# Kernel tuning notes

Hardware: AMD Instinct MI355X
Metric: run time of the kernel (lower is better)

The kernel has to match this reference:

```python
import jax, jax.numpy as jnp
import numpy as np

DIM = 1024
N_HEAD = 16
N_KV_HEAD = 4
HEAD_DIM = DIM // N_HEAD  # 64
INTER = 2688
B, N = 2, 2048
EPS = 1e-6


def setup_inputs() -> dict:
    key = jax.random.key(0)
    ks = jax.random.split(key, 10)
    std = 0.02
    x = jax.random.normal(ks[0], (B, N, DIM), dtype=jnp.float32)
    # rotary embedding: theta = pos * 10000^(-2i/d), cos/sin of shape [N, HEAD_DIM//2]
    inv_freq = 1.0 / (10000.0 ** (np.arange(0, HEAD_DIM, 2, dtype=np.float32) / HEAD_DIM))
    t = np.arange(N, dtype=np.float32)
    ang = np.outer(t, inv_freq)  # [N, HEAD_DIM//2]
    rope_cos = jnp.asarray(np.cos(ang))
    rope_sin = jnp.asarray(np.sin(ang))
    mask = jnp.tril(jnp.ones((N, N), dtype=bool))  # True = attend
    return {
        "x": x,
        "w_attn_norm": jnp.ones((DIM,), jnp.float32),
        "w_ffn_norm": jnp.ones((DIM,), jnp.float32),
        "Wq": jax.random.normal(ks[1], (DIM, N_HEAD * HEAD_DIM), jnp.float32) * std,
        "Wkv": jax.random.normal(ks[2], (DIM, 2 * N_KV_HEAD * HEAD_DIM), jnp.float32) * std,
        "Wo": jax.random.normal(ks[3], (N_HEAD * HEAD_DIM, DIM), jnp.float32) * std,
        "W1": jax.random.normal(ks[4], (DIM, INTER), jnp.float32) * std,
        "W2": jax.random.normal(ks[5], (INTER, DIM), jnp.float32) * std,
        "W3": jax.random.normal(ks[6], (DIM, INTER), jnp.float32) * std,
        "rope_cos": rope_cos,
        "rope_sin": rope_sin,
        "mask": mask,
    }


def _rms_norm(x, w):
    # nn.functional.rms_norm: x / sqrt(mean(x^2) + eps) * w
    return x * jax.lax.rsqrt(jnp.mean(x * x, axis=-1, keepdims=True) + EPS) * w


def _apply_rope(x, cos, sin):
    # x: [b, n, h, d]; consecutive pairs (x[2k], x[2k+1]) form complex numbers
    xr = x[..., 0::2]
    xi = x[..., 1::2]
    c = cos[None, :, None, :]
    s = sin[None, :, None, :]
    yr = xr * c - xi * s
    yi = xr * s + xi * c
    return jnp.stack([yr, yi], axis=-1).reshape(x.shape)


def _block(x, w_attn_norm, w_ffn_norm, Wq, Wkv, Wo, W1, W2, W3, rope_cos, rope_sin, mask):
    b, n, _ = x.shape
    # --- attention (GQA, use_cache=False prefill) ---
    h = _rms_norm(x, w_attn_norm)
    q = (h @ Wq).reshape(b, n, N_HEAD, HEAD_DIM)
    kv = h @ Wkv
    k, v = jnp.split(kv, 2, axis=-1)
    k = k.reshape(b, n, N_KV_HEAD, HEAD_DIM)
    v = v.reshape(b, n, N_KV_HEAD, HEAD_DIM)
    q = _apply_rope(q, rope_cos, rope_sin)
    k = _apply_rope(k, rope_cos, rope_sin)
    # einops repeat 'b n h d -> b n (r h) d' == tile along head axis
    r = N_HEAD // N_KV_HEAD
    k = jnp.tile(k, (1, 1, r, 1))
    v = jnp.tile(v, (1, 1, r, 1))
    scale = HEAD_DIM ** -0.5
    scores = jnp.einsum('bnhd,bmhd->bhnm', q, k) * scale
    scores = jnp.where(mask[None, None, :, :], scores, jnp.finfo(scores.dtype).min)
    attn = jax.nn.softmax(scores, axis=-1)
    o = jnp.einsum('bhnm,bmhd->bnhd', attn, v).reshape(b, n, N_HEAD * HEAD_DIM)
    x = x + o @ Wo
    # --- SwiGLU MLP ---
    h2 = _rms_norm(x, w_ffn_norm)
    ff = (jax.nn.silu(h2 @ W1) * (h2 @ W3)) @ W2
    return x + ff


def reference(x, w_attn_norm, w_ffn_norm, Wq, Wkv, Wo, W1, W2, W3, rope_cos, rope_sin, mask):
    return _block(x, w_attn_norm, w_ffn_norm, Wq, Wkv, Wo, W1, W2, W3, rope_cos, rope_sin, mask)
```

## Files before the change

kernel.cpp:

```cpp
#include <hip/hip_runtime.h>

#define DIM 1024
#define NH 16
#define NKV 4
#define HD 64
#define INTER 2688
#define BB 2
#define NN 2048
#define MM (BB*NN)

typedef __attribute__((ext_vector_type(4))) float f32x4;
typedef __attribute__((ext_vector_type(16))) float f32x16;
typedef __attribute__((ext_vector_type(8))) short short8;

#define CROW(r,h) ((((r)&3)) + 8*((r)>>2) + 4*(h))

__device__ __forceinline__ unsigned short f2bf(float f) {
  union { float f; unsigned u; } v; v.f = f;
  unsigned r = v.u + 0x7fffu + ((v.u >> 16) & 1u);
  return (unsigned short)(r >> 16);
}

__device__ __forceinline__ void glds16(const unsigned short* g, unsigned short* l) {
  __builtin_amdgcn_global_load_lds(
      (const __attribute__((address_space(1))) void*)g,
      (__attribute__((address_space(3))) void*)l, 16, 0, 0);
}

__device__ __forceinline__ void xcd_map(int& bx, int& by) {
  int gx = gridDim.x;
  int nwg = gx * gridDim.y;
  int bid = (int)blockIdx.y * gx + (int)blockIdx.x;
  int cpx = nwg >> 3;
  int lg = (bid & 7) * cpx + (bid >> 3);
  bx = lg % gx;
  by = lg / gx;
}

__global__ void transpose_all(const float* __restrict__ Wq, const float* __restrict__ Wkv,
                              const float* __restrict__ Wo, const float* __restrict__ W1,
                              const float* __restrict__ W3, const float* __restrict__ W2,
                              unsigned short* __restrict__ WqkvT, unsigned short* __restrict__ WoT,
                              unsigned short* __restrict__ W1T, unsigned short* __restrict__ W3T,
                              unsigned short* __restrict__ W2T) {
  int tb = blockIdx.x;
  const float* src; unsigned short* dst; int K, Nc, t0;
  if (tb < 1024)        { src = Wq;  dst = WqkvT;                         K = 1024; Nc = 1024; t0 = tb; }
  else if (tb < 1536)   { src = Wkv; dst = WqkvT + (size_t)1024 * 1024;   K = 1024; Nc = 512;  t0 = tb - 1024; }
  else if (tb < 2560)   { src = Wo;  dst = WoT;                           K = 1024; Nc = 1024; t0 = tb - 1536; }
  else if (tb < 5248)   { src = W1;  dst = W1T;                           K = 1024; Nc = 2688; t0 = tb - 2560; }
  else if (tb < 7936)   { src = W3;  dst = W3T;                           K = 1024; Nc = 2688; t0 = tb - 5248; }
  else                  { src = W2;  dst = W2T;                           K = 2688; Nc = 1024; t0 = tb - 7936; }
  int ntx = Nc >> 5;
  int n0 = (t0 % ntx) * 32, k0 = (t0 / ntx) * 32;
  __shared__ float tile[32][33];
  int tx = threadIdx.x & 31, ty = threadIdx.x >> 5;
#pragma unroll
  for (int i = 0; i < 32; i += 8)
    tile[ty + i][tx] = src[(size_t)(k0 + ty + i) * Nc + n0 + tx];
  __syncthreads();
#pragma unroll
  for (int i = 0; i < 32; i += 8)
    dst[(size_t)(n0 + ty + i) * K + k0 + tx] = f2bf(tile[tx][ty + i]);
}

__global__ void rmsnorm_k(const float* __restrict__ x, const float* __restrict__ w,
                          unsigned short* __restrict__ h) {
  int row = blockIdx.x;
  int t = threadIdx.x;
  const float4* xr = (const float4*)(x + (size_t)row * DIM);
  float4 v = xr[t];
  float ss = v.x * v.x + v.y * v.y + v.z * v.z + v.w * v.w;
#pragma unroll
  for (int o = 1; o < 64; o <<= 1) ss += __shfl_xor(ss, o);
  __shared__ float ps[4];
  if ((t & 63) == 0) ps[t >> 6] = ss;
  __syncthreads();
  float r = rsqrtf((ps[0] + ps[1] + ps[2] + ps[3]) * (1.0f / DIM) + 1e-6f);
  const float4* wr = (const float4*)w;
  float4 wv = wr[t];
  ushort4 o4;
  o4.x = f2bf(v.x * r * wv.x);
  o4.y = f2bf(v.y * r * wv.y);
  o4.z = f2bf(v.z * r * wv.z);
  o4.w = f2bf(v.w * r * wv.w);
  *(ushort4*)(h + (size_t)row * DIM + t * 4) = o4;
}

template <bool RES>
__global__ __launch_bounds__(256, 3) void gemm_f32(
    const unsigned short* __restrict__ A, const unsigned short* __restrict__ Bt,
    const float* __restrict__ res, float* __restrict__ C, int Nc, int K) {
  __shared__ __align__(16) unsigned short Asm[3][128 * 32];
  __shared__ __align__(16) unsigned short Bsm[3][128 * 32];
  int tid = threadIdx.x;
  int w = tid >> 6, l = tid & 63;
  int bx, by;
  xcd_map(bx, by);
  int bm = by * 128, bn = bx * 128;
  int wr = (w >> 1) * 64, wc = (w & 1) * 64;
  int c0 = l & 15, g = l >> 4;

  int sr = w * 32 + (l >> 2);
  int sc = ((l & 3) ^ ((sr >> 1) & 3)) * 8;
  const unsigned short* gA0 = A + (size_t)(bm + sr) * K + sc;
  const unsigned short* gA1 = A + (size_t)(bm + sr + 16) * K + sc;
  const unsigned short* gB0 = Bt + (size_t)(bn + sr) * K + sc;
  const unsigned short* gB1 = Bt + (size_t)(bn + sr + 16) * K + sc;
  int ls0 = (w * 32) * 32, ls1 = (w * 32 + 16) * 32;

  int aoff[4], boff[4];
#pragma unroll
  for (int m = 0; m < 4; m++) {
    int ra = wr + m * 16 + c0;
    aoff[m] = ra * 32 + (g ^ ((ra >> 1) & 3)) * 8;
    int rb = wc + m * 16 + c0;
    boff[m] = rb * 32 + (g ^ ((rb >> 1) & 3)) * 8;
  }

  f32x4 acc[4][4] = {};
  int T = K / 32;
  glds16(gA0, &Asm[0][ls0]);
  glds16(gA1, &Asm[0][ls1]);
  glds16(gB0, &Bsm[0][ls0]);
  glds16(gB1, &Bsm[0][ls1]);
  glds16(gA0 + 32, &Asm[1][ls0]);
  glds16(gA1 + 32, &Asm[1][ls1]);
  glds16(gB0 + 32, &Bsm[1][ls0]);
  glds16(gB1 + 32, &Bsm[1][ls1]);
  int cur = 0;
  for (int t = 0; t < T; ++t) {
    if (t + 2 < T) {
      int nx = cur + 2; if (nx >= 3) nx -= 3;
      int ko = (t + 2) * 32;
      glds16(gA0 + ko, &Asm[nx][ls0]);
      glds16(gA1 + ko, &Asm[nx][ls1]);
      glds16(gB0 + ko, &Bsm[nx][ls0]);
      glds16(gB1 + ko, &Bsm[nx][ls1]);
      asm volatile("s_waitcnt vmcnt(8)" ::: "memory");
    } else if (t + 2 == T) {
      asm volatile("s_waitcnt vmcnt(4)" ::: "memory");
    } else {
      asm volatile("s_waitcnt vmcnt(0)" ::: "memory");
    }
    __builtin_amdgcn_s_barrier();
    __builtin_amdgcn_sched_barrier(0);
    const unsigned short* As = Asm[cur];
    const unsigned short* Bs = Bsm[cur];
    short8 af[4], bf[4];
#pragma unroll
    for (int m = 0; m < 4; m++) af[m] = *(const short8*)&As[aoff[m]];
#pragma unroll
    for (int n = 0; n < 4; n++) bf[n] = *(const short8*)&Bs[boff[n]];
    __builtin_amdgcn_s_setprio(1);
#pragma unroll
    for (int m = 0; m < 4; m++)
#pragma unroll
      for (int n = 0; n < 4; n++)
        acc[m][n] = __builtin_amdgcn_mfma_f32_16x16x32_bf16(af[m], bf[n], acc[m][n], 0, 0, 0);
    __builtin_amdgcn_s_setprio(0);
    asm volatile("s_waitcnt lgkmcnt(0)" ::: "memory");
    __builtin_amdgcn_sched_barrier(0);
    __builtin_amdgcn_s_barrier();
    cur = cur + 1 == 3 ? 0 : cur + 1;
  }
  int gq = l >> 4;
#pragma unroll
  for (int m = 0; m < 4; m++) {
#pragma unroll
    for (int i = 0; i < 4; i++) {
      int row = bm + wr + m * 16 + gq * 4 + i;
#pragma unroll
      for (int n = 0; n < 4; n++) {
        int col = bn + wc + n * 16 + c0;
        float v = acc[m][n][i];
        if (RES) v += res[(size_t)row * Nc + col];
        C[(size_t)row * Nc + col] = v;
      }
    }
  }
}

__global__ __launch_bounds__(256, 3) void gemm_qkv(
    const unsigned short* __restrict__ A, const unsigned short* __restrict__ Bt,
    const float* __restrict__ cosb, const float* __restrict__ sinb,
    unsigned short* __restrict__ qb, unsigned short* __restrict__ kb,
    unsigned short* __restrict__ vtb) {
  const int Nc = 1536, K = 1024;
  const float QS = 0.125f * 1.44269504f;
  __shared__ __align__(16) unsigned short Asm[3][128 * 32];
  __shared__ __align__(16) unsigned short Bsm[3][128 * 32];
  int tid = threadIdx.x;
  int w = tid >> 6, l = tid & 63;
  int bx, by;
  xcd_map(bx, by);
  int bm = by * 128, bn = bx * 128;
  int wr = (w >> 1) * 64, wc = (w & 1) * 64;
  int c0 = l & 15, g = l >> 4;

  int sr = w * 32 + (l >> 2);
  int sc = ((l & 3) ^ ((sr >> 1) & 3)) * 8;
  const unsigned short* gA0 = A + (size_t)(bm + sr) * K + sc;
  const unsigned short* gA1 = A + (size_t)(bm + sr + 16) * K + sc;
  const unsigned short* gB0 = Bt + (size_t)(bn + sr) * K + sc;
  const unsigned short* gB1 = Bt + (size_t)(bn + sr + 16) * K + sc;
  int ls0 = (w * 32) * 32, ls1 = (w * 32 + 16) * 32;

  int aoff[4], boff[4];
#pragma unroll
  for (int m = 0; m < 4; m++) {
    int ra = wr + m * 16 + c0;
    aoff[m] = ra * 32 + (g ^ ((ra >> 1) & 3)) * 8;
    int rb = wc + m * 16 + c0;
    boff[m] = rb * 32 + (g ^ ((rb >> 1) & 3)) * 8;
  }

  f32x4 acc[4][4] = {};
  int T = K / 32;
  glds16(gA0, &Asm[0][ls0]);
  glds16(gA1, &Asm[0][ls1]);
  glds16(gB0, &Bsm[0][ls0]);
  glds16(gB1, &Bsm[0][ls1]);
  glds16(gA0 + 32, &Asm[1][ls0]);
  glds16(gA1 + 32, &Asm[1][ls1]);
  glds16(gB0 + 32, &Bsm[1][ls0]);
  glds16(gB1 + 32, &Bsm[1][ls1]);
  int cur = 0;
  for (int t = 0; t < T; ++t) {
    if (t + 2 < T) {
      int nx = cur + 2; if (nx >= 3) nx -= 3;
      int ko = (t + 2) * 32;
      glds16(gA0 + ko, &Asm[nx][ls0]);
      glds16(gA1 + ko, &Asm[nx][ls1]);
      glds16(gB0 + ko, &Bsm[nx][ls0]);
      glds16(gB1 + ko, &Bsm[nx][ls1]);
      asm volatile("s_waitcnt vmcnt(8)" ::: "memory");
    } else if (t + 2 == T) {
      asm volatile("s_waitcnt vmcnt(4)" ::: "memory");
    } else {
      asm volatile("s_waitcnt vmcnt(0)" ::: "memory");
    }
    __builtin_amdgcn_s_barrier();
    __builtin_amdgcn_sched_barrier(0);
    const unsigned short* As = Asm[cur];
    const unsigned short* Bs = Bsm[cur];
    short8 af[4], bf[4];
#pragma unroll
    for (int m = 0; m < 4; m++) af[m] = *(const short8*)&As[aoff[m]];
#pragma unroll
    for (int n = 0; n < 4; n++) bf[n] = *(const short8*)&Bs[boff[n]];
    __builtin_amdgcn_s_setprio(1);
#pragma unroll
    for (int m = 0; m < 4; m++)
#pragma unroll
      for (int n = 0; n < 4; n++)
        acc[m][n] = __builtin_amdgcn_mfma_f32_16x16x32_bf16(af[m], bf[n], acc[m][n], 0, 0, 0);
    __builtin_amdgcn_s_setprio(0);
    asm volatile("s_waitcnt lgkmcnt(0)" ::: "memory");
    __builtin_amdgcn_sched_barrier(0);
    __builtin_amdgcn_s_barrier();
    cur = cur + 1 == 3 ? 0 : cur + 1;
  }
  int gq = l >> 4;
  int lodd = c0 & 1;
#pragma unroll
  for (int m = 0; m < 4; m++) {
#pragma unroll
    for (int i = 0; i < 4; i++) {
      int row = bm + wr + m * 16 + gq * 4 + i;
      int b = row >> 11, tok = row & (NN - 1);
#pragma unroll
      for (int n = 0; n < 4; n++) {
        int col = bn + wc + n * 16 + c0;
        float val = acc[m][n][i];
        float partner = __shfl_xor(val, 1);
        if (bn < 1024) {
          int head = col >> 6, d = col & 63, j = d >> 1;
          float c = cosb[tok * 32 + j], s = sinb[tok * 32 + j];
          float r = lodd ? (partner * s + val * c) : (val * c - partner * s);
          qb[(((size_t)(b * NH + head)) * NN + tok) * 64 + d] = f2bf(r * QS);
        } else if (bn < 1280) {
          int cc = col - 1024;
          int kvh = cc >> 6, d = cc & 63, j = d >> 1;
          float c = cosb[tok * 32 + j], s = sinb[tok * 32 + j];
          float r = lodd ? (partner * s + val * c) : (val * c - partner * s);
          kb[(((size_t)(b * NKV + kvh)) * NN + tok) * 64 + d] = f2bf(r);
        } else {
          int cc = col - 1280;
          int kvh = cc >> 6, d = cc & 63;
          vtb[(((size_t)(b * NKV + kvh)) * 64 + d) * NN + tok] = f2bf(val);
        }
      }
    }
  }
}

__global__ __launch_bounds__(256, 3) void gemm_ffn13(
    const unsigned short* __restrict__ A, const unsigned short* __restrict__ B1t,
    const unsigned short* __restrict__ B3t, unsigned short* __restrict__ G,
    int Nc, int K) {
  __shared__ __align__(16) unsigned short Asm[2 * 128 * 32];
  __shared__ __align__(16) unsigned short B1sm[2 * 64 * 32];
  __shared__ __align__(16) unsigned short B3sm[2 * 64 * 32];
  int tid = threadIdx.x;
  int w = tid >> 6, l = tid & 63;
  int bx, by;
  xcd_map(bx, by);
  int bm = by * 128, bn = bx * 64;
  int wr = (w >> 1) * 64, wc = (w & 1) * 32;
  int c0 = l & 15, g = l >> 4;

  int sr = w * 32 + (l >> 2);
  int sb = w * 16 + (l >> 2);
  int sc  = ((l & 3) ^ ((sr >> 1) & 3)) * 8;
  int scb = ((l & 3) ^ ((sb >> 1) & 3)) * 8;
  const unsigned short* gA0 = A + (size_t)(bm + sr) * K + sc;
  const unsigned short* gA1 = A + (size_t)(bm + sr + 16) * K + sc;
  const unsigned short* gB1 = B1t + (size_t)(bn + sb) * K + scb;
  const unsigned short* gB3 = B3t + (size_t)(bn + sb) * K + scb;
  int ls0 = (w * 32) * 32, ls1 = (w * 32 + 16) * 32, lsb = (w * 16) * 32;

  int aoff[4], boff[2];
#pragma unroll
  for (int m = 0; m < 4; m++) {
    int ra = wr + m * 16 + c0;
    aoff[m] = ra * 32 + (g ^ ((ra >> 1) & 3)) * 8;
  }
#pragma unroll
  for (int n = 0; n < 2; n++) {
    int rb = wc + n * 16 + c0;
    boff[n] = rb * 32 + (g ^ ((rb >> 1) & 3)) * 8;
  }

  f32x4 a1[4][2] = {};
  f32x4 a3[4][2] = {};
  int nsteps = K / 32;
  glds16(gA0, &Asm[ls0]);
  glds16(gA1, &Asm[ls1]);
  glds16(gB1, &B1sm[lsb]);
  glds16(gB3, &B3sm[lsb]);
  __syncthreads();
  int buf = 0;
  for (int s = 0; s < nsteps; ++s) {
    int nb = buf ^ 1;
    if (s + 1 < nsteps) {
      int ko = (s + 1) * 32;
      glds16(gA0 + ko, &Asm[nb * 4096 + ls0]);
      glds16(gA1 + ko, &Asm[nb * 4096 + ls1]);
      glds16(gB1 + ko, &B1sm[nb * 2048 + lsb]);
      glds16(gB3 + ko, &B3sm[nb * 2048 + lsb]);
    }
    const unsigned short* As = &Asm[buf * 4096];
    const unsigned short* B1s = &B1sm[buf * 2048];
    const unsigned short* B3s = &B3sm[buf * 2048];
    short8 af[4], b1f[2], b3f[2];
#pragma unroll
    for (int m = 0; m < 4; m++) af[m] = *(const short8*)&As[aoff[m]];
#pragma unroll
    for (int n = 0; n < 2; n++) {
      b1f[n] = *(const short8*)&B1s[boff[n]];
      b3f[n] = *(const short8*)&B3s[boff[n]];
    }
    __builtin_amdgcn_s_setprio(1);
#pragma unroll
    for (int m = 0; m < 4; m++)
#pragma unroll
      for (int n = 0; n < 2; n++) {
        a1[m][n] = __builtin_amdgcn_mfma_f32_16x16x32_bf16(af[m], b1f[n], a1[m][n], 0, 0, 0);
        a3[m][n] = __builtin_amdgcn_mfma_f32_16x16x32_bf16(af[m], b3f[n], a3[m][n], 0, 0, 0);
      }
    __builtin_amdgcn_s_setprio(0);
    __syncthreads();
    buf = nb;
  }
  int gq = l >> 4;
#pragma unroll
  for (int m = 0; m < 4; m++) {
#pragma unroll
    for (int i = 0; i < 4; i++) {
      int row = bm + wr + m * 16 + gq * 4 + i;
#pragma unroll
      for (int n = 0; n < 2; n++) {
        int col = bn + wc + n * 16 + c0;
        float x1 = a1[m][n][i], x3 = a3[m][n][i];
        float sg = x1 / (1.0f + __expf(-x1));
        G[(size_t)row * Nc + col] = f2bf(sg * x3);
      }
    }
  }
}

__global__ __launch_bounds__(256, 3) void attn_k(
    const unsigned short* __restrict__ qg_, const unsigned short* __restrict__ kg_,
    const unsigned short* __restrict__ vg_, unsigned short* __restrict__ ob) {
  __shared__ __align__(16) unsigned short Ksm[2][64 * 64];
  __shared__ __align__(16) unsigned short Vsm[2][64 * 64];
  int qb = (blockIdx.z == 0) ? (int)blockIdx.x : ((int)gridDim.x - 1 - (int)blockIdx.x);
  int h = blockIdx.y, b = blockIdx.z;
  int kvh = h & 3;
  int tid = threadIdx.x, w = tid >> 6, l = tid & 63;
  int q5 = l & 31, hi = l >> 5;
  int qwbase = qb * 128 + w * 32;
  int qgl = qwbase + q5;

  const unsigned short* Kg = kg_ + ((size_t)(b * NKV + kvh)) * NN * 64;
  const unsigned short* Vg = vg_ + ((size_t)(b * NKV + kvh)) * 64 * NN;

  short8 qf[4];
  {
    const unsigned short* qrow = qg_ + (((size_t)(b * NH + h)) * NN + qgl) * 64 + hi * 8;
#pragma unroll
    for (int d = 0; d < 4; d++) qf[d] = *(const short8*)(qrow + d * 16);
  }

  int srow = l >> 3;
  int schunk = (l & 7) ^ (srow & 7);
  const unsigned short* gK = Kg + (size_t)(w * 16 + srow) * 64 + schunk * 8;
  const unsigned short* gV = Vg + (size_t)(w * 16 + srow) * NN + schunk * 8;

  int nkt = qb * 2 + 2;
  int nkt_w = ((qwbase + 31) >> 6) + 1;

  f32x16 O0 = {}, O1 = {};
  float m_r = -1e30f, l_r = 0.0f;

  glds16(gK, &Ksm[0][w * 1024]);
  glds16(gK + 8 * 64, &Ksm[0][w * 1024 + 512]);
  glds16(gV, &Vsm[0][w * 1024]);
  glds16(gV + 8 * NN, &Vsm[0][w * 1024 + 512]);
  __syncthreads();

  int buf = 0;
  for (int kt = 0; kt < nkt; ++kt) {
    int n0 = kt * 64;
    if (kt + 1 < nkt) {
      int nb = buf ^ 1;
      glds16(gK + (size_t)(n0 + 64) * 64, &Ksm[nb][w * 1024]);
      glds16(gK + (size_t)(n0 + 64) * 64 + 8 * 64, &Ksm[nb][w * 1024 + 512]);
      glds16(gV + n0 + 64, &Vsm[nb][w * 1024]);
      glds16(gV + 8 * NN + n0 + 64, &Vsm[nb][w * 1024 + 512]);
    }
    if (kt < nkt_w) {
      const unsigned short* Ks = Ksm[buf];
      const unsigned short* Vs = Vsm[buf];
      f32x16 S[2];
      __builtin_amdgcn_s_setprio(1);
#pragma unroll
      for (int s = 0; s < 2; s++) {
        f32x16 acc = {};
        int row = s * 32 + q5;
#pragma unroll
        for (int d = 0; d < 4; d++) {
          int ch = (2 * d + hi) ^ (row & 7);
          short8 kf = *(const short8*)&Ks[row * 64 + ch * 8];
          acc = __builtin_amdgcn_mfma_f32_32x32x16_bf16(kf, qf[d], acc, 0, 0, 0);
        }
        S[s] = acc;
      }
      __builtin_amdgcn_s_setprio(0);
      if (kt == nkt_w - 1) {
#pragma unroll
        for (int s = 0; s < 2; s++)
#pragma unroll
          for (int r = 0; r < 16; r++) {
            int kg = n0 + s * 32 + CROW(r, hi);
            S[s][r] = (kg > qgl) ? -1e30f : S[s][r];
          }
      }
      float t16[16];
#pragma unroll
      for (int r = 0; r < 16; r++) t16[r] = fmaxf(S[0][r], S[1][r]);
#pragma unroll
      for (int k = 8; k >= 1; k >>= 1)
#pragma unroll
        for (int r = 0; r < k; r++) t16[r] = fmaxf(t16[r], t16[r + k]);
      float pm = fmaxf(t16[0], __shfl_xor(t16[0], 32));
      if (!__all(pm <= m_r + 8.0f)) {
        float mn = fmaxf(m_r, pm);
        float alpha = exp2f(m_r - mn);
        m_r = mn;
        l_r *= alpha;
        float ab[16];
#pragma unroll
        for (int r = 0; r < 16; r++) ab[r] = __shfl(alpha, CROW(r, 0) + 4 * hi);
#pragma unroll
        for (int r = 0; r < 16; r++) { O0[r] *= ab[r]; O1[r] *= ab[r]; }
      }
#pragma unroll
      for (int s = 0; s < 2; s++)
#pragma unroll
        for (int r = 0; r < 16; r++) S[s][r] = exp2f(S[s][r] - m_r);
      float u[16];
#pragma unroll
      for (int r = 0; r < 16; r++) u[r] = S[0][r] + S[1][r];
#pragma unroll
      for (int k = 8; k >= 1; k >>= 1)
#pragma unroll
        for (int r = 0; r < k; r++) u[r] += u[r + k];
      l_r += (u[0] + __shfl_xor(u[0], 32));
      short8 paf[4];
#pragma unroll
      for (int ks = 0; ks < 4; ks++) {
        const int s = ks >> 1, e = ks & 1;
        unsigned a0, a1, b0, b1;
        asm("v_cvt_pk_bf16_f32 %0, %1, %2" : "=v"(a0) : "v"(S[s][8*e+0]), "v"(S[s][8*e+1]));
        asm("v_cvt_pk_bf16_f32 %0, %1, %2" : "=v"(a1) : "v"(S[s][8*e+2]), "v"(S[s][8*e+3]));
        asm("v_cvt_pk_bf16_f32 %0, %1, %2" : "=v"(b0) : "v"(S[s][8*e+4]), "v"(S[s][8*e+5]));
        asm("v_cvt_pk_bf16_f32 %0, %1, %2" : "=v"(b1) : "v"(S[s][8*e+6]), "v"(S[s][8*e+7]));
        asm("v_permlane32_swap_b32 %0, %1" : "+v"(a0), "+v"(b0));
        asm("v_permlane32_swap_b32 %0, %1" : "+v"(a1), "+v"(b1));
        union { unsigned u4[4]; short8 s8; } pk;
        pk.u4[0] = a0; pk.u4[1] = a1; pk.u4[2] = b0; pk.u4[3] = b1;
        paf[ks] = pk.s8;
      }
      __builtin_amdgcn_s_setprio(1);
#pragma unroll
      for (int ks = 0; ks < 4; ks++) {
        int row0 = q5, row1 = 32 + q5;
        short8 vf0 = *(const short8*)&Vs[row0 * 64 + (((2 * ks + hi) ^ (row0 & 7)) * 8)];
        short8 vf1 = *(const short8*)&Vs[row1 * 64 + (((2 * ks + hi) ^ (row1 & 7)) * 8)];
        O0 = __builtin_amdgcn_mfma_f32_32x32x16_bf16(paf[ks], vf0, O0, 0, 0, 0);
        O1 = __builtin_amdgcn_mfma_f32_32x32x16_bf16(paf[ks], vf1, O1, 0, 0, 0);
      }
      __builtin_amdgcn_s_setprio(0);
    }
    __syncthreads();
    buf ^= 1;
  }
  float linv = 1.0f / l_r;
  float lb[16];
#pragma unroll
  for (int r = 0; r < 16; r++) lb[r] = __shfl(linv, CROW(r, 0) + 4 * hi);
#pragma unroll
  for (int r = 0; r < 16; r++) {
    int orow = qwbase + CROW(r, hi);
    size_t base = ((size_t)b * NN + orow) * 1024 + h * 64 + q5;
    ob[base] = f2bf(O0[r] * lb[r]);
    ob[base + 32] = f2bf(O1[r] * lb[r]);
  }
}

extern "C" void kernel_launch(void* const* d_in, const int* in_sizes, int n_in,
                              void* d_out, int out_size, void* d_ws, size_t ws_size,
                              hipStream_t stream) {
  (void)in_sizes; (void)n_in; (void)out_size; (void)ws_size;
  const float* x    = (const float*)d_in[0];
  const float* w_an = (const float*)d_in[1];
  const float* w_fn = (const float*)d_in[2];
  const float* Wq   = (const float*)d_in[3];
  const float* Wkv  = (const float*)d_in[4];
  const float* Wo   = (const float*)d_in[5];
  const float* W1   = (const float*)d_in[6];
  const float* W2   = (const float*)d_in[7];
  const float* W3   = (const float*)d_in[8];
  const float* cosb = (const float*)d_in[9];
  const float* sinb = (const float*)d_in[10];
  float* out = (float*)d_out;

  char* ws = (char*)d_ws;
  size_t off = 0;
  auto take = [&](size_t bytes) {
    size_t r = off;
    off += (bytes + 255) & ~(size_t)255;
    return r;
  };
  unsigned short* WqkvT = (unsigned short*)(ws + take((size_t)1536 * 1024 * 2));
  unsigned short* WoT   = (unsigned short*)(ws + take((size_t)1024 * 1024 * 2));
  unsigned short* W1T   = (unsigned short*)(ws + take((size_t)2688 * 1024 * 2));
  unsigned short* W3T   = (unsigned short*)(ws + take((size_t)2688 * 1024 * 2));
  unsigned short* W2T   = (unsigned short*)(ws + take((size_t)2688 * 1024 * 2));
  unsigned short* hA    = (unsigned short*)(ws + take((size_t)MM * DIM * 2));
  unsigned short* gbuf  = (unsigned short*)(ws + take((size_t)MM * INTER * 2));
  unsigned short* qbuf = (unsigned short*)(ws + take((size_t)MM * DIM * 2));
  unsigned short* kbuf = (unsigned short*)(ws + take((size_t)BB * NKV * NN * HD * 2));
  unsigned short* vtb  = (unsigned short*)(ws + take((size_t)BB * NKV * NN * HD * 2));
  unsigned short* obuf = (unsigned short*)(ws + take((size_t)MM * DIM * 2));
  float* x2 = (float*)(ws + take((size_t)MM * DIM * 4));

  transpose_all<<<10624, 256, 0, stream>>>(Wq, Wkv, Wo, W1, W3, W2,
                                           WqkvT, WoT, W1T, W3T, W2T);
  rmsnorm_k<<<MM, 256, 0, stream>>>(x, w_an, hA);
  gemm_qkv<<<dim3(1536 / 128, MM / 128), 256, 0, stream>>>(hA, WqkvT, cosb, sinb,
                                                           qbuf, kbuf, vtb);
  attn_k<<<dim3(NN / 128, NH, BB), 256, 0, stream>>>(qbuf, kbuf, vtb, obuf);
  gemm_f32<true><<<dim3(1024 / 128, MM / 128), 256, 0, stream>>>(obuf, WoT, x, x2, 1024, 1024);
  rmsnorm_k<<<MM, 256, 0, stream>>>(x2, w_fn, hA);
  gemm_ffn13<<<dim3(INTER / 64, MM / 128), 256, 0, stream>>>(hA, W1T, W3T, gbuf, INTER, 1024);
  gemm_f32<true><<<dim3(1024 / 128, MM / 128), 256, 0, stream>>>(gbuf, W2T, x2, out, 1024, 2688);
}
```

Before: 260.3 us.

## Use 64x128 tiles with double buffering for QKV, Wo and W2 GEMMs

```diff
diff --git a/kernel.cpp b/kernel.cpp
--- a/kernel.cpp
+++ b/kernel.cpp
@@ -88,90 +88,80 @@
 }
 
 template <bool RES>
-__global__ __launch_bounds__(256, 3) void gemm_f32(
+__global__ __launch_bounds__(256, 4) void gemm64(
     const unsigned short* __restrict__ A, const unsigned short* __restrict__ Bt,
     const float* __restrict__ res, float* __restrict__ C, int Nc, int K) {
-  __shared__ __align__(16) unsigned short Asm[3][128 * 32];
-  __shared__ __align__(16) unsigned short Bsm[3][128 * 32];
+  __shared__ __align__(16) unsigned short Asm[2][64 * 32];
+  __shared__ __align__(16) unsigned short Bsm[2][128 * 32];
   int tid = threadIdx.x;
   int w = tid >> 6, l = tid & 63;
   int bx, by;
   xcd_map(bx, by);
-  int bm = by * 128, bn = bx * 128;
-  int wr = (w >> 1) * 64, wc = (w & 1) * 64;
+  int bm = by * 64, bn = bx * 128;
+  int wc = w * 32;
   int c0 = l & 15, g = l >> 4;
 
-  int sr = w * 32 + (l >> 2);
-  int sc = ((l & 3) ^ ((sr >> 1) & 3)) * 8;
-  const unsigned short* gA0 = A + (size_t)(bm + sr) * K + sc;
-  const unsigned short* gA1 = A + (size_t)(bm + sr + 16) * K + sc;
-  const unsigned short* gB0 = Bt + (size_t)(bn + sr) * K + sc;
-  const unsigned short* gB1 = Bt + (size_t)(bn + sr + 16) * K + sc;
-  int ls0 = (w * 32) * 32, ls1 = (w * 32 + 16) * 32;
-
-  int aoff[4], boff[4];
+  int sra = w * 16 + (l >> 2);
+  int srb = w * 32 + (l >> 2);
+  int sca = ((l & 3) ^ ((sra >> 1) & 3)) * 8;
+  int scb = ((l & 3) ^ ((srb >> 1) & 3)) * 8;
+  const unsigned short* gA  = A + (size_t)(bm + sra) * K + sca;
+  const unsigned short* gB0 = Bt + (size_t)(bn + srb) * K + scb;
+  const unsigned short* gB1 = Bt + (size_t)(bn + srb + 16) * K + scb;
+  int lsa = (w * 16) * 32, lsb0 = (w * 32) * 32, lsb1 = (w * 32 + 16) * 32;
+
+  int aoff[4], boff[2];
 #pragma unroll
   for (int m = 0; m < 4; m++) {
-    int ra = wr + m * 16 + c0;
+    int ra = m * 16 + c0;
     aoff[m] = ra * 32 + (g ^ ((ra >> 1) & 3)) * 8;
-    int rb = wc + m * 16 + c0;
-    boff[m] = rb * 32 + (g ^ ((rb >> 1) & 3)) * 8;
-  }
-
-  f32x4 acc[4][4] = {};
+  }
+#pragma unroll
+  for (int n = 0; n < 2; n++) {
+    int rb = wc + n * 16 + c0;
+    boff[n] = rb * 32 + (g ^ ((rb >> 1) & 3)) * 8;
+  }
+
+  f32x4 acc[4][2] = {};
   int T = K / 32;
-  glds16(gA0, &Asm[0][ls0]);
-  glds16(gA1, &Asm[0][ls1]);
-  glds16(gB0, &Bsm[0][ls0]);
-  glds16(gB1, &Bsm[0][ls1]);
-  glds16(gA0 + 32, &Asm[1][ls0]);
-  glds16(gA1 + 32, &Asm[1][ls1]);
-  glds16(gB0 + 32, &Bsm[1][ls0]);
-  glds16(gB1 + 32, &Bsm[1][ls1]);
-  int cur = 0;
-  for (int t = 0; t < T; ++t) {
-    if (t + 2 < T) {
-      int nx = cur + 2; if (nx >= 3) nx -= 3;
-      int ko = (t + 2) * 32;
-      glds16(gA0 + ko, &Asm[nx][ls0]);
-      glds16(gA1 + ko, &Asm[nx][ls1]);
-      glds16(gB0 + ko, &Bsm[nx][ls0]);
-      glds16(gB1 + ko, &Bsm[nx][ls1]);
-      asm volatile("s_waitcnt vmcnt(8)" ::: "memory");
-    } else if (t + 2 == T) {
-      asm volatile("s_waitcnt vmcnt(4)" ::: "memory");
-    } else {
-      asm volatile("s_waitcnt vmcnt(0)" ::: "memory");
-    }
-    __builtin_amdgcn_s_barrier();
-    __builtin_amdgcn_sched_barrier(0);
-    const unsigned short* As = Asm[cur];
-    const unsigned short* Bs = Bsm[cur];
-    short8 af[4], bf[4];
+  glds16(gA, &Asm[0][lsa]);
+  glds16(gB0, &Bsm[0][lsb0]);
+  glds16(gB1, &Bsm[0][lsb1]);
+  __syncthreads();
+  int buf = 0;
+  for (int s = 0; s < T; ++s) {
+    int nb = buf ^ 1;
+    if (s + 1 < T) {
+      int ko = (s + 1) * 32;
+      glds16(gA + ko, &Asm[nb][lsa]);
+      glds16(gB0 + ko, &Bsm[nb][lsb0]);
+      glds16(gB1 + ko, &Bsm[nb][lsb1]);
+    }
+    const unsigned short* As = Asm[buf];
+    const unsigned short* Bs = Bsm[buf];
+    short8 af[4], bf[2];
 #pragma unroll
     for (int m = 0; m < 4; m++) af[m] = *(const short8*)&As[aoff[m]];
 #pragma unroll
-    for (int n = 0; n < 4; n++) bf[n] = *(const short8*)&Bs[boff[n]];
+    for (int n = 0; n < 2; n++) bf[n] = *(const short8*)&Bs[boff[n]];
     __builtin_amdgcn_s_setprio(1);
 #pragma unroll
     for (int m = 0; m < 4; m++)
 #pragma unroll
-      for (int n = 0; n < 4; n++)
+      for (int n = 0; n < 2; n++)
         acc[m][n] = __builtin_amdgcn_mfma_f32_16x16x32_bf16(af[m], bf[n], acc[m][n], 0, 0, 0);
     __builtin_amdgcn_s_setprio(0);
-    asm volatile("s_waitcnt lgkmcnt(0)" ::: "memory");
-    __builtin_amdgcn_sched_barrier(0);
-    __builtin_amdgcn_s_barrier();
-    cur = cur + 1 == 3 ? 0 : cur + 1;
+    __syncthreads();
+    buf = nb;
   }
   int gq = l >> 4;
 #pragma unroll
   for (int m = 0; m < 4; m++) {
 #pragma unroll
     for (int i = 0; i < 4; i++) {
-      int row = bm + wr + m * 16 + gq * 4 + i;
-#pragma unroll
-      for (int n = 0; n < 4; n++) {
+      int row = bm + m * 16 + gq * 4 + i;
+#pragma unroll
+      for (int n = 0; n < 2; n++) {
         int col = bn + wc + n * 16 + c0;
         float v = acc[m][n][i];
         if (RES) v += res[(size_t)row * Nc + col];
@@ -181,85 +171,75 @@
   }
 }
 
-__global__ __launch_bounds__(256, 3) void gemm_qkv(
+__global__ __launch_bounds__(256, 4) void gemm_qkv(
     const unsigned short* __restrict__ A, const unsigned short* __restrict__ Bt,
     const float* __restrict__ cosb, const float* __restrict__ sinb,
     unsigned short* __restrict__ qb, unsigned short* __restrict__ kb,
     unsigned short* __restrict__ vtb) {
-  const int Nc = 1536, K = 1024;
+  const int K = 1024;
   const float QS = 0.125f * 1.44269504f;
-  __shared__ __align__(16) unsigned short Asm[3][128 * 32];
-  __shared__ __align__(16) unsigned short Bsm[3][128 * 32];
+  __shared__ __align__(16) unsigned short Asm[2][64 * 32];
+  __shared__ __align__(16) unsigned short Bsm[2][128 * 32];
   int tid = threadIdx.x;
   int w = tid >> 6, l = tid & 63;
   int bx, by;
   xcd_map(bx, by);
-  int bm = by * 128, bn = bx * 128;
-  int wr = (w >> 1) * 64, wc = (w & 1) * 64;
+  int bm = by * 64, bn = bx * 128;
+  int wc = w * 32;
   int c0 = l & 15, g = l >> 4;
 
-  int sr = w * 32 + (l >> 2);
-  int sc = ((l & 3) ^ ((sr >> 1) & 3)) * 8;
-  const unsigned short* gA0 = A + (size_t)(bm + sr) * K + sc;
-  const unsigned short* gA1 = A + (size_t)(bm + sr + 16) * K + sc;
-  const unsigned short* gB0 = Bt + (size_t)(bn + sr) * K + sc;
-  const unsigned short* gB1 = Bt + (size_t)(bn + sr + 16) * K + sc;
-  int ls0 = (w * 32) * 32, ls1 = (w * 32 + 16) * 32;
-
-  int aoff[4], boff[4];
+  int sra = w * 16 + (l >> 2);
+  int srb = w * 32 + (l >> 2);
+  int sca = ((l & 3) ^ ((sra >> 1) & 3)) * 8;
+  int scb = ((l & 3) ^ ((srb >> 1) & 3)) * 8;
+  const unsigned short* gA  = A + (size_t)(bm + sra) * K + sca;
+  const unsigned short* gB0 = Bt + (size_t)(bn + srb) * K + scb;
+  const unsigned short* gB1 = Bt + (size_t)(bn + srb + 16) * K + scb;
+  int lsa = (w * 16) * 32, lsb0 = (w * 32) * 32, lsb1 = (w * 32 + 16) * 32;
+
+  int aoff[4], boff[2];
 #pragma unroll
   for (int m = 0; m < 4; m++) {
-    int ra = wr + m * 16 + c0;
+    int ra = m * 16 + c0;
     aoff[m] = ra * 32 + (g ^ ((ra >> 1) & 3)) * 8;
-    int rb = wc + m * 16 + c0;
-    boff[m] = rb * 32 + (g ^ ((rb >> 1) & 3)) * 8;
-  }
-
-  f32x4 acc[4][4] = {};
+  }
+#pragma unroll
+  for (int n = 0; n < 2; n++) {
+    int rb = wc + n * 16 + c0;
+    boff[n] = rb * 32 + (g ^ ((rb >> 1) & 3)) * 8;
+  }
+
+  f32x4 acc[4][2] = {};
   int T = K / 32;
-  glds16(gA0, &Asm[0][ls0]);
-  glds16(gA1, &Asm[0][ls1]);
-  glds16(gB0, &Bsm[0][ls0]);
-  glds16(gB1, &Bsm[0][ls1]);
-  glds16(gA0 + 32, &Asm[1][ls0]);
-  glds16(gA1 + 32, &Asm[1][ls1]);
-  glds16(gB0 + 32, &Bsm[1][ls0]);
-  glds16(gB1 + 32, &Bsm[1][ls1]);
-  int cur = 0;
-  for (int t = 0; t < T; ++t) {
-    if (t + 2 < T) {
-      int nx = cur + 2; if (nx >= 3) nx -= 3;
-      int ko = (t + 2) * 32;
-      glds16(gA0 + ko, &Asm[nx][ls0]);
-      glds16(gA1 + ko, &Asm[nx][ls1]);
-      glds16(gB0 + ko, &Bsm[nx][ls0]);
-      glds16(gB1 + ko, &Bsm[nx][ls1]);
-      asm volatile("s_waitcnt vmcnt(8)" ::: "memory");
-    } else if (t + 2 == T) {
-      asm volatile("s_waitcnt vmcnt(4)" ::: "memory");
-    } else {
-      asm volatile("s_waitcnt vmcnt(0)" ::: "memory");
-    }
-    __builtin_amdgcn_s_barrier();
-    __builtin_amdgcn_sched_barrier(0);
-    const unsigned short* As = Asm[cur];
-    const unsigned short* Bs = Bsm[cur];
-    short8 af[4], bf[4];
+  glds16(gA, &Asm[0][lsa]);
+  glds16(gB0, &Bsm[0][lsb0]);
+  glds16(gB1, &Bsm[0][lsb1]);
+  __syncthreads();
+  int buf = 0;
+  for (int s = 0; s < T; ++s) {
+    int nb = buf ^ 1;
+    if (s + 1 < T) {
+      int ko = (s + 1) * 32;
+      glds16(gA + ko, &Asm[nb][lsa]);
+      glds16(gB0 + ko, &Bsm[nb][lsb0]);
+      glds16(gB1 + ko, &Bsm[nb][lsb1]);
+    }
+    const unsigned short* As = Asm[buf];
+    const unsigned short* Bs = Bsm[buf];
+    short8 af[4], bf[2];
 #pragma unroll
     for (int m = 0; m < 4; m++) af[m] = *(const short8*)&As[aoff[m]];
 #pragma unroll
-    for (int n = 0; n < 4; n++) bf[n] = *(const short8*)&Bs[boff[n]];
+    for (int n = 0; n < 2; n++) bf[n] = *(const short8*)&Bs[boff[n]];
     __builtin_amdgcn_s_setprio(1);
 #pragma unroll
     for (int m = 0; m < 4; m++)
 #pragma unroll
-      for (int n = 0; n < 4; n++)
+      for (int n = 0; n < 2; n++)
         acc[m][n] = __builtin_amdgcn_mfma_f32_16x16x32_bf16(af[m], bf[n], acc[m][n], 0, 0, 0);
     __builtin_amdgcn_s_setprio(0);
-    asm volatile("s_waitcnt lgkmcnt(0)" ::: "memory");
-    __builtin_amdgcn_sched_barrier(0);
-    __builtin_amdgcn_s_barrier();
-    cur = cur + 1 == 3 ? 0 : cur + 1;
+    __syncthreads();
+    buf = nb;
   }
   int gq = l >> 4;
   int lodd = c0 & 1;
@@ -267,10 +247,10 @@
   for (int m = 0; m < 4; m++) {
 #pragma unroll
     for (int i = 0; i < 4; i++) {
-      int row = bm + wr + m * 16 + gq * 4 + i;
+      int row = bm + m * 16 + gq * 4 + i;
       int b = row >> 11, tok = row & (NN - 1);
 #pragma unroll
-      for (int n = 0; n < 4; n++) {
+      for (int n = 0; n < 2; n++) {
         int col = bn + wc + n * 16 + c0;
         float val = acc[m][n][i];
         float partner = __shfl_xor(val, 1);
@@ -304,9 +284,7 @@
   __shared__ __align__(16) unsigned short B3sm[2 * 64 * 32];
   int tid = threadIdx.x;
   int w = tid >> 6, l = tid & 63;
-  int bx, by;
-  xcd_map(bx, by);
-  int bm = by * 128, bn = bx * 64;
+  int bm = blockIdx.y * 128, bn = blockIdx.x * 64;
   int wr = (w >> 1) * 64, wc = (w & 1) * 32;
   int c0 = l & 15, g = l >> 4;
 
@@ -580,11 +558,11 @@
   transpose_all<<<10624, 256, 0, stream>>>(Wq, Wkv, Wo, W1, W3, W2,
                                            WqkvT, WoT, W1T, W3T, W2T);
   rmsnorm_k<<<MM, 256, 0, stream>>>(x, w_an, hA);
-  gemm_qkv<<<dim3(1536 / 128, MM / 128), 256, 0, stream>>>(hA, WqkvT, cosb, sinb,
-                                                           qbuf, kbuf, vtb);
+  gemm_qkv<<<dim3(1536 / 128, MM / 64), 256, 0, stream>>>(hA, WqkvT, cosb, sinb,
+                                                          qbuf, kbuf, vtb);
   attn_k<<<dim3(NN / 128, NH, BB), 256, 0, stream>>>(qbuf, kbuf, vtb, obuf);
-  gemm_f32<true><<<dim3(1024 / 128, MM / 128), 256, 0, stream>>>(obuf, WoT, x, x2, 1024, 1024);
+  gemm64<true><<<dim3(1024 / 128, MM / 64), 256, 0, stream>>>(obuf, WoT, x, x2, 1024, 1024);
   rmsnorm_k<<<MM, 256, 0, stream>>>(x2, w_fn, hA);
   gemm_ffn13<<<dim3(INTER / 64, MM / 128), 256, 0, stream>>>(hA, W1T, W3T, gbuf, INTER, 1024);
-  gemm_f32<true><<<dim3(1024 / 128, MM / 128), 256, 0, stream>>>(gbuf, W2T, x2, out, 1024, 2688);
-}
+  gemm64<true><<<dim3(1024 / 128, MM / 64), 256, 0, stream>>>(gbuf, W2T, x2, out, 1024, 2688);
+}
```

Measured after the change: 238.4 us. -8.4%, faster.
